# Kernel optimization log

Hardware: AMD Instinct MI355X
Metric: run time of the kernel (lower is better)

## Reference

```python
import jax, jax.numpy as jnp
import numpy as np

BANDWIDTH_SQ = 1.0   # h^2 = bandwidth**2, bandwidth=1.0
EPS = 0.0            # clamp floor before log (module default)


def setup_inputs() -> dict:
    key = jax.random.key(0)
    k1, k2, k3 = jax.random.split(key, 3)
    X = jax.random.normal(k1, (2048, 16), dtype=jnp.float32)
    data = jax.random.normal(k2, (100000, 16), dtype=jnp.float32)
    sample_weight = jax.random.uniform(k3, (100000,), dtype=jnp.float32)
    return {"X": X, "data": data, "sample_weight": sample_weight}


def reference(X, data, sample_weight):
    # Brute-force ('standard' RootTree returns all points) weighted Gaussian KDE.
    d = X.shape[1]
    # squared distances [Q, N] via expansion (avoids [Q, N, d] intermediate)
    sq = (
        jnp.sum(X * X, axis=-1)[:, None]
        + jnp.sum(data * data, axis=-1)[None, :]
        - 2.0 * (X @ data.T)
    )
    kernel_values = jnp.exp(-0.5 * sq / BANDWIDTH_SQ)  # [Q, N]
    norm_constant = (2.0 * jnp.pi * BANDWIDTH_SQ) ** (-d / 2.0)
    density = (kernel_values @ sample_weight) * norm_constant / jnp.sum(sample_weight)
    log_density = jnp.log(jnp.maximum(density, EPS))
    return log_density
```

## Files before the change

kernel.cpp:

```cpp
#include <hip/hip_runtime.h>

#define D 16
#define WQT 1
#define NCHUNK 192
#define TILES_MAX 33
#define FIN_QPB 64

#define LOG2E 1.4426950408889634f
#define LN2   0.6931471805599453f

typedef __attribute__((ext_vector_type(8))) short bf16x8;
typedef __attribute__((ext_vector_type(4))) float f32x4;

__device__ __forceinline__ unsigned short f2bf(float f) {
    unsigned u = __float_as_uint(f);
    unsigned r = (u + 0x7fffu + ((u >> 16) & 1u)) >> 16;
    return (unsigned short)r;
}

__global__ __launch_bounds__(256, 8) void dens_kernel(
        const float* __restrict__ X, const float* __restrict__ data,
        const float* __restrict__ w, float* __restrict__ part,
        float* __restrict__ wpart, int Q, int N) {
    __shared__ unsigned short sh_hi[(TILES_MAX + 1) * 256];
    __shared__ float          sh_cn[(TILES_MAX + 1) * 16];
    __shared__ float          ls[4];

    const int lane = threadIdx.x & 63;
    const int wave = threadIdx.x >> 6;
    const int col  = lane & 15;
    const int quad = lane >> 4;
    const int koff = (quad & 1) * 8;

    const int qg = blockIdx.x * 4 + wave;

    const int NT = N >> 4;
    const int base = NT / NCHUNK, rem = NT % NCHUNK;
    const int chunk = blockIdx.y;
    const int tile0 = chunk * base + min(chunk, rem);
    const int cnt = base + (chunk < rem ? 1 : 0);
    const int npts = cnt * 16;
    const int n0 = tile0 * 16;

    float ws = 0.f;
    for (int p = threadIdx.x; p < npts; p += 256) {
        const float4* dp = (const float4*)(data + (size_t)(n0 + p) * D);
        float4 v0 = dp[0], v1 = dp[1], v2 = dp[2], v3 = dp[3];
        float vv[16] = {v0.x, v0.y, v0.z, v0.w, v1.x, v1.y, v1.z, v1.w,
                        v2.x, v2.y, v2.z, v2.w, v3.x, v3.y, v3.z, v3.w};
        float dd = 0.f;
        unsigned hp[8];
        #pragma unroll
        for (int j = 0; j < 8; j++) {
            float a = vv[2 * j], b = vv[2 * j + 1];
            dd = fmaf(a, a, fmaf(b, b, dd));
            hp[j] = (unsigned)f2bf(a) | ((unsigned)f2bf(b) << 16);
        }
        uint4* dst = (uint4*)(sh_hi + p * 16);
        dst[0] = make_uint4(hp[0], hp[1], hp[2], hp[3]);
        dst[1] = make_uint4(hp[4], hp[5], hp[6], hp[7]);
        float wn = w[n0 + p];
        ws += wn;
        sh_cn[p] = fmaf(-0.5f * LOG2E, dd, __builtin_amdgcn_logf(wn));
    }
    #pragma unroll
    for (int off = 32; off > 0; off >>= 1) ws += __shfl_down(ws, off, 64);
    if (lane == 0) ls[wave] = ws;

    bf16x8 afrag[WQT];
    #pragma unroll
    for (int t = 0; t < WQT; t++) {
        int q = (qg * WQT + t) * 16 + col;
        const float* xp = X + (size_t)q * D + koff;
        bf16x8 a;
        #pragma unroll
        for (int j = 0; j < 8; j++)
            a[j] = (quad < 2) ? (short)f2bf(xp[j] * LOG2E) : (short)0;
        afrag[t] = a;
    }

    f32x4 dens[WQT];
    #pragma unroll
    for (int t = 0; t < WQT; t++) dens[t] = (f32x4){0.f, 0.f, 0.f, 0.f};

    __syncthreads();

    if (threadIdx.x == 0)
        wpart[chunk] = (ls[0] + ls[1]) + (ls[2] + ls[3]);

    const int eoff = (col << 4) + koff;
    bf16x8 b1 = *(const bf16x8*)(sh_hi + eoff);
    float  c0 = sh_cn[col];
    #pragma unroll 2
    for (int it = 0; it < cnt; it++) {
        bf16x8 nb1 = *(const bf16x8*)(sh_hi + (it + 1) * 256 + eoff);
        float  nc0 = sh_cn[(it + 1) * 16 + col];
        f32x4 cvec = {c0, c0, c0, c0};
        #pragma unroll
        for (int t = 0; t < WQT; t++) {
            f32x4 s = __builtin_amdgcn_mfma_f32_16x16x32_bf16(afrag[t], b1, cvec, 0, 0, 0);
            f32x4 e;
            #pragma unroll
            for (int r = 0; r < 4; r++)
                e[r] = __builtin_amdgcn_exp2f(s[r]);
            dens[t] += e;
        }
        b1 = nb1; c0 = nc0;
    }

    #pragma unroll
    for (int t = 0; t < WQT; t++) {
        #pragma unroll
        for (int r = 0; r < 4; r++) {
            float v = dens[t][r];
            v += __shfl_xor(v, 1, 64);
            v += __shfl_xor(v, 2, 64);
            v += __shfl_xor(v, 4, 64);
            v += __shfl_xor(v, 8, 64);
            if (col == 0) {
                int q = (qg * WQT + t) * 16 + quad * 4 + r;
                part[(size_t)chunk * Q + q] = v;
            }
        }
    }
}

__global__ __launch_bounds__(192) void fin_kernel(
        const float* __restrict__ X, const float* __restrict__ part,
        const float* __restrict__ wpart, float* __restrict__ out, int Q) {
    __shared__ float sred[3][FIN_QPB];
    __shared__ float swsum;

    const int tid = threadIdx.x;
    const int qi = tid & (FIN_QPB - 1);
    const int seg = tid >> 6;
    const int q = blockIdx.x * FIN_QPB + qi;

    float a0 = 0.f, a1 = 0.f, a2 = 0.f, a3 = 0.f;
    const int c0 = seg * 64;
    #pragma unroll 4
    for (int c = 0; c < 64; c += 4) {
        a0 += part[(size_t)(c0 + c + 0) * Q + q];
        a1 += part[(size_t)(c0 + c + 1) * Q + q];
        a2 += part[(size_t)(c0 + c + 2) * Q + q];
        a3 += part[(size_t)(c0 + c + 3) * Q + q];
    }
    sred[seg][qi] = (a0 + a1) + (a2 + a3);

    if (tid < 64) {
        float wv = wpart[tid] + wpart[tid + 64] + wpart[tid + 128];
        #pragma unroll
        for (int off = 32; off > 0; off >>= 1) wv += __shfl_down(wv, off, 64);
        if (tid == 0) swsum = wv;
    }
    __syncthreads();

    if (tid < FIN_QPB) {
        float dsum = sred[0][tid] + sred[1][tid] + sred[2][tid];
        int qq = blockIdx.x * FIN_QPB + tid;
        const float4* xp = (const float4*)(X + (size_t)qq * D);
        float4 x0 = xp[0], x1 = xp[1], x2 = xp[2], x3 = xp[3];
        float xx = x0.x*x0.x + x0.y*x0.y + x0.z*x0.z + x0.w*x0.w
                 + x1.x*x1.x + x1.y*x1.y + x1.z*x1.z + x1.w*x1.w
                 + x2.x*x2.x + x2.y*x2.y + x2.z*x2.z + x2.w*x2.w
                 + x3.x*x3.x + x3.y*x3.y + x3.z*x3.z + x3.w*x3.w;
        float aq = -0.5f * LOG2E * xx;
        const float ln_norm = -8.f * 1.8378770664093453f;
        out[qq] = LN2 * (aq + __builtin_amdgcn_logf(dsum)
                            - __builtin_amdgcn_logf(swsum)) + ln_norm;
    }
}

extern "C" void kernel_launch(void* const* d_in, const int* in_sizes, int n_in,
                              void* d_out, int out_size, void* d_ws, size_t ws_size,
                              hipStream_t stream) {
    const float* X    = (const float*)d_in[0];
    const float* data = (const float*)d_in[1];
    const float* w    = (const float*)d_in[2];
    float* out = (float*)d_out;
    int Q = in_sizes[0] / D;
    int N = in_sizes[1] / D;

    float* wpart = (float*)d_ws;
    float* part  = wpart + NCHUNK;

    dim3 grid(Q / (4 * WQT * 16), NCHUNK);
    dens_kernel<<<grid, 256, 0, stream>>>(X, data, w, part, wpart, Q, N);

    fin_kernel<<<Q / FIN_QPB, 192, 0, stream>>>(X, part, wpart, out, Q);
}
```

Before: 107.7 us.

## Switch density kernel to 32x32x16 bf16 MFMA with split-K LDS planes

Replaces the 16x16x32 MFMA, whose K dimension was half zero-padded for D=16, with a 32x32x16 MFMA that uses the full K=16. Data points are now tiled in groups of 32 and stored in two LDS planes, one per half of the feature dimension, so each lane loads its 8-element K slice contiguously. Each wave now handles 32 queries. The number of data chunks rises from 192 to 256, and the finalize kernel is widened to reduce four segments. The goal is to remove wasted matrix-core work and cut per-tile loop overhead. The cost is more accumulator registers per lane and a changed grid shape.

```diff
diff --git a/kernel.cpp b/kernel.cpp
--- a/kernel.cpp
+++ b/kernel.cpp
@@ -1,16 +1,17 @@
 #include <hip/hip_runtime.h>
 
 #define D 16
-#define WQT 1
-#define NCHUNK 192
-#define TILES_MAX 33
+#define NCH 256
+#define TILES_MAX 13
 #define FIN_QPB 64
 
 #define LOG2E 1.4426950408889634f
 #define LN2   0.6931471805599453f
 
-typedef __attribute__((ext_vector_type(8))) short bf16x8;
-typedef __attribute__((ext_vector_type(4))) float f32x4;
+#define PLANE ((TILES_MAX + 1) * 32 * 8)
+
+typedef __attribute__((ext_vector_type(8)))  short bf16x8;
+typedef __attribute__((ext_vector_type(16))) float f32x16;
 
 __device__ __forceinline__ unsigned short f2bf(float f) {
     unsigned u = __float_as_uint(f);
@@ -22,25 +23,24 @@
         const float* __restrict__ X, const float* __restrict__ data,
         const float* __restrict__ w, float* __restrict__ part,
         float* __restrict__ wpart, int Q, int N) {
-    __shared__ unsigned short sh_hi[(TILES_MAX + 1) * 256];
-    __shared__ float          sh_cn[(TILES_MAX + 1) * 16];
+    __shared__ unsigned short sh_hi[2 * PLANE];
+    __shared__ float          sh_cn[(TILES_MAX + 1) * 32];
     __shared__ float          ls[4];
 
-    const int lane = threadIdx.x & 63;
-    const int wave = threadIdx.x >> 6;
-    const int col  = lane & 15;
-    const int quad = lane >> 4;
-    const int koff = (quad & 1) * 8;
+    const int lane  = threadIdx.x & 63;
+    const int wave  = threadIdx.x >> 6;
+    const int col32 = lane & 31;
+    const int khalf = lane >> 5;
 
     const int qg = blockIdx.x * 4 + wave;
 
-    const int NT = N >> 4;
-    const int base = NT / NCHUNK, rem = NT % NCHUNK;
+    const int NT = N >> 5;
+    const int base = NT / NCH, rem = NT % NCH;
     const int chunk = blockIdx.y;
     const int tile0 = chunk * base + min(chunk, rem);
     const int cnt = base + (chunk < rem ? 1 : 0);
-    const int npts = cnt * 16;
-    const int n0 = tile0 * 16;
+    const int npts = cnt * 32;
+    const int n0 = tile0 * 32;
 
     float ws = 0.f;
     for (int p = threadIdx.x; p < npts; p += 256) {
@@ -56,9 +56,8 @@
             dd = fmaf(a, a, fmaf(b, b, dd));
             hp[j] = (unsigned)f2bf(a) | ((unsigned)f2bf(b) << 16);
         }
-        uint4* dst = (uint4*)(sh_hi + p * 16);
-        dst[0] = make_uint4(hp[0], hp[1], hp[2], hp[3]);
-        dst[1] = make_uint4(hp[4], hp[5], hp[6], hp[7]);
+        *(uint4*)(sh_hi + p * 8)         = make_uint4(hp[0], hp[1], hp[2], hp[3]);
+        *(uint4*)(sh_hi + PLANE + p * 8) = make_uint4(hp[4], hp[5], hp[6], hp[7]);
         float wn = w[n0 + p];
         ws += wn;
         sh_cn[p] = fmaf(-0.5f * LOG2E, dd, __builtin_amdgcn_logf(wn));
@@ -67,68 +66,60 @@
     for (int off = 32; off > 0; off >>= 1) ws += __shfl_down(ws, off, 64);
     if (lane == 0) ls[wave] = ws;
 
-    bf16x8 afrag[WQT];
-    #pragma unroll
-    for (int t = 0; t < WQT; t++) {
-        int q = (qg * WQT + t) * 16 + col;
-        const float* xp = X + (size_t)q * D + koff;
-        bf16x8 a;
+    bf16x8 afrag;
+    {
+        int q = qg * 32 + col32;
+        const float* xp = X + (size_t)q * D + khalf * 8;
         #pragma unroll
         for (int j = 0; j < 8; j++)
-            a[j] = (quad < 2) ? (short)f2bf(xp[j] * LOG2E) : (short)0;
-        afrag[t] = a;
+            afrag[j] = (short)f2bf(xp[j] * LOG2E);
     }
 
-    f32x4 dens[WQT];
+    f32x16 dens;
     #pragma unroll
-    for (int t = 0; t < WQT; t++) dens[t] = (f32x4){0.f, 0.f, 0.f, 0.f};
+    for (int r = 0; r < 16; r++) dens[r] = 0.f;
 
     __syncthreads();
 
     if (threadIdx.x == 0)
         wpart[chunk] = (ls[0] + ls[1]) + (ls[2] + ls[3]);
 
-    const int eoff = (col << 4) + koff;
+    const int eoff = khalf * PLANE + col32 * 8;
     bf16x8 b1 = *(const bf16x8*)(sh_hi + eoff);
-    float  c0 = sh_cn[col];
+    float  c0 = sh_cn[col32];
     #pragma unroll 2
     for (int it = 0; it < cnt; it++) {
         bf16x8 nb1 = *(const bf16x8*)(sh_hi + (it + 1) * 256 + eoff);
-        float  nc0 = sh_cn[(it + 1) * 16 + col];
-        f32x4 cvec = {c0, c0, c0, c0};
+        float  nc0 = sh_cn[(it + 1) * 32 + col32];
+        f32x16 s;
         #pragma unroll
-        for (int t = 0; t < WQT; t++) {
-            f32x4 s = __builtin_amdgcn_mfma_f32_16x16x32_bf16(afrag[t], b1, cvec, 0, 0, 0);
-            f32x4 e;
-            #pragma unroll
-            for (int r = 0; r < 4; r++)
-                e[r] = __builtin_amdgcn_exp2f(s[r]);
-            dens[t] += e;
-        }
+        for (int r = 0; r < 16; r++) s[r] = c0;
+        s = __builtin_amdgcn_mfma_f32_32x32x16_bf16(afrag, b1, s, 0, 0, 0);
+        #pragma unroll
+        for (int r = 0; r < 16; r++)
+            dens[r] += __builtin_amdgcn_exp2f(s[r]);
         b1 = nb1; c0 = nc0;
     }
 
     #pragma unroll
-    for (int t = 0; t < WQT; t++) {
-        #pragma unroll
-        for (int r = 0; r < 4; r++) {
-            float v = dens[t][r];
-            v += __shfl_xor(v, 1, 64);
-            v += __shfl_xor(v, 2, 64);
-            v += __shfl_xor(v, 4, 64);
-            v += __shfl_xor(v, 8, 64);
-            if (col == 0) {
-                int q = (qg * WQT + t) * 16 + quad * 4 + r;
-                part[(size_t)chunk * Q + q] = v;
-            }
+    for (int r = 0; r < 16; r++) {
+        float v = dens[r];
+        v += __shfl_xor(v, 1, 64);
+        v += __shfl_xor(v, 2, 64);
+        v += __shfl_xor(v, 4, 64);
+        v += __shfl_xor(v, 8, 64);
+        v += __shfl_xor(v, 16, 64);
+        if (col32 == 0) {
+            int q = qg * 32 + (r & 3) + 8 * (r >> 2) + 4 * khalf;
+            part[(size_t)chunk * Q + q] = v;
         }
     }
 }
 
-__global__ __launch_bounds__(192) void fin_kernel(
+__global__ __launch_bounds__(256) void fin_kernel(
         const float* __restrict__ X, const float* __restrict__ part,
         const float* __restrict__ wpart, float* __restrict__ out, int Q) {
-    __shared__ float sred[3][FIN_QPB];
+    __shared__ float sred[4][FIN_QPB];
     __shared__ float swsum;
 
     const int tid = threadIdx.x;
@@ -148,7 +139,8 @@
     sred[seg][qi] = (a0 + a1) + (a2 + a3);
 
     if (tid < 64) {
-        float wv = wpart[tid] + wpart[tid + 64] + wpart[tid + 128];
+        float wv = (wpart[tid] + wpart[tid + 64])
+                 + (wpart[tid + 128] + wpart[tid + 192]);
         #pragma unroll
         for (int off = 32; off > 0; off >>= 1) wv += __shfl_down(wv, off, 64);
         if (tid == 0) swsum = wv;
@@ -156,7 +148,7 @@
     __syncthreads();
 
     if (tid < FIN_QPB) {
-        float dsum = sred[0][tid] + sred[1][tid] + sred[2][tid];
+        float dsum = (sred[0][tid] + sred[1][tid]) + (sred[2][tid] + sred[3][tid]);
         int qq = blockIdx.x * FIN_QPB + tid;
         const float4* xp = (const float4*)(X + (size_t)qq * D);
         float4 x0 = xp[0], x1 = xp[1], x2 = xp[2], x3 = xp[3];
@@ -182,10 +174,10 @@
     int N = in_sizes[1] / D;
 
     float* wpart = (float*)d_ws;
-    float* part  = wpart + NCHUNK;
+    float* part  = wpart + NCH;
 
-    dim3 grid(Q / (4 * WQT * 16), NCHUNK);
+    dim3 grid(Q / (4 * 32), NCH);
     dens_kernel<<<grid, 256, 0, stream>>>(X, data, w, part, wpart, Q, N);
 
-    fin_kernel<<<Q / FIN_QPB, 192, 0, stream>>>(X, part, wpart, out, Q);
+    fin_kernel<<<Q / FIN_QPB, 256, 0, stream>>>(X, part, wpart, out, Q);
 }
```

Result: faster. 96.58 us (-10.3%).
